# Kernel optimization log

Hardware: AMD Instinct MI355X
Metric: run time of the kernel (lower is better)

Reference implementation:

```python
import jax, jax.numpy as jnp
import numpy as np

B, N, N_IN, N_H = 8192, 16, 512, 256
NEG_ROUND = 1
MARGIN = 0.5
EPS = 1e-6  # torch F.pairwise_distance default eps


def setup_inputs() -> dict:
    key = jax.random.key(0)
    k0, k1, k2, k3 = jax.random.split(key, 4)
    seq1 = jax.random.normal(k0, (B, N, N_IN), dtype=jnp.float32)
    adj = jax.random.uniform(k1, (B, N, N), dtype=jnp.float32)
    # GCN linear (bias=False), xavier_uniform on [n_h, n_in] == same bound for [n_in, n_h]
    gx = float(np.sqrt(6.0 / (N_IN + N_H)))
    W_gcn = jax.random.uniform(k2, (N_IN, N_H), dtype=jnp.float32, minval=-gx, maxval=gx)
    b_gcn = jnp.zeros((N_H,), dtype=jnp.float32)  # Simple_GCN self.bias, init 0
    prelu_a = jnp.asarray(0.25, dtype=jnp.float32)  # nn.PReLU default
    bx = float(np.sqrt(6.0 / (N_H + N_H)))
    W_bil = jax.random.uniform(k3, (N_H, N_H), dtype=jnp.float32, minval=-bx, maxval=bx)
    b_bil = jnp.zeros((), dtype=jnp.float32)
    return {"seq1": seq1, "adj": adj, "W_gcn": W_gcn, "b_gcn": b_gcn,
            "prelu_a": prelu_a, "W_bil": W_bil, "b_bil": b_bil}


def reference(seq1, adj, W_gcn, b_gcn, prelu_a, W_bil, b_bil):
    # Simple_GCN: linear -> adjacency aggregate -> bias -> PReLU
    seq_fts = jnp.einsum('bnf,fh->bnh', seq1, W_gcn)           # [B,N,n_h]
    h1 = jnp.einsum('bnm,bmh->bnh', adj, seq_fts) + b_gcn      # bmm(adj, seq_fts)+bias
    h1 = jnp.where(h1 >= 0, h1, prelu_a * h1)                  # PReLU

    # avg readout over context nodes; last node is the target
    c = jnp.mean(h1[:, :-1, :], axis=1)                        # [B,n_h]
    h_mv = h1[:, -1, :]                                        # [B,n_h]

    def bilinear(x1, x2):  # nn.Bilinear(n_h, n_h, 1)
        return jnp.einsum('bi,ij,bj->b', x1, W_bil, x2)[:, None] + b_bil  # [B,1]

    scs = [bilinear(h_mv, c)]
    c_mi = c
    for _ in range(NEG_ROUND):  # fixed small loop, mirrors torch shift
        c_mi = jnp.concatenate([c_mi[-2:-1, :], c_mi[:-1, :]], axis=0)
        scs.append(bilinear(h_mv, c_mi))

    pos_dis = jnp.linalg.norm(h_mv - c + EPS, axis=-1)         # F.pairwise_distance
    neg_dis = jnp.linalg.norm(h_mv - c_mi + EPS, axis=-1)

    logits = jnp.concatenate(scs, axis=0)                      # [(1+NEG)*B, 1]
    # MarginRankingLoss(margin, reduction='none') with y=-1:
    # max(0, -y*(x1-x2)+margin) = max(0, (pos-neg)+margin)
    loss2 = jnp.maximum(0.0, (pos_dis - neg_dis) + MARGIN)     # [B]
    return (logits, loss2)
```

## Files before the change

kernel.cpp:

```cpp
#include <hip/hip_runtime.h>
#include <stdint.h>

typedef float f32x4 __attribute__((ext_vector_type(4)));
typedef __bf16 bfrag __attribute__((ext_vector_type(8)));
typedef unsigned short us4 __attribute__((ext_vector_type(4)));

__device__ __forceinline__ unsigned short f2bf(float f) {
  unsigned u = __float_as_uint(f);
  u += 0x7fff + ((u >> 16) & 1);
  return (unsigned short)(u >> 16);
}
__device__ __forceinline__ float bf2f(unsigned short s) {
  return __uint_as_float(((unsigned)s) << 16);
}

typedef __attribute__((address_space(3))) void lds_vp;
typedef __attribute__((address_space(1))) void gl_vp;
__device__ __forceinline__ void gload16(const void* g, void* l) {
  __builtin_amdgcn_global_load_lds((const gl_vp*)g, (lds_vp*)l, 16, 0, 0);
}

__global__ __launch_bounds__(256)
void conv_w_k(const float* __restrict__ Wg, const float* __restrict__ Wb,
              unsigned short* __restrict__ WgT, unsigned short* __restrict__ WbT) {
  int i = blockIdx.x * 256 + threadIdx.x;
  if (i < 512 * 256) { int k = i >> 8, c = i & 255; WgT[c * 512 + k] = f2bf(Wg[i]); }
  if (i < 256 * 256) { int k = i >> 8, c = i & 255; WbT[c * 256 + k] = f2bf(Wb[i]); }
}

__global__ __launch_bounds__(512, 4)
void fused1_k(const float* __restrict__ A, const unsigned short* __restrict__ Bt,
              const float* __restrict__ adj, const float* __restrict__ b_gcn,
              const float* __restrict__ prelu_a,
              float* __restrict__ Cout, float* __restrict__ Hmv) {
  __shared__ __align__(16) char sm[65536];
  const int t = threadIdx.x;
  const int lane = t & 63;
  const int wid = t >> 6;
  const int wm = wid >> 2, wn = wid & 3;
  const int lrow = lane & 15, lgrp = lane >> 4;
  const int wg = blockIdx.x;

  const float* gA = A + (size_t)(wg * 128 + (t >> 2)) * 512 + (t & 3) * 8;
  const int aw_off = t * 16;

  int aoff[4], boff[4];
#pragma unroll
  for (int m = 0; m < 4; m++) {
    int arow = wm * 64 + m * 16 + lrow;
    aoff[m] = arow * 64 + lgrp * 16;
  }
#pragma unroll
  for (int n = 0; n < 4; n++) {
    int bcol = wn * 64 + n * 16 + lrow;
    boff[n] = 8192 + bcol * 64 + ((lgrp ^ ((bcol ^ (bcol >> 2)) & 3)) << 4);
  }

  f32x4 acc[4][4];
#pragma unroll
  for (int m = 0; m < 4; m++)
#pragma unroll
    for (int n = 0; n < 4; n++) acc[m][n] = (f32x4)0.0f;

#define STAGE_B(buf, kc)                                                       \
  {                                                                            \
    _Pragma("unroll")                                                          \
    for (int i = 0; i < 2; i++) {                                              \
      int c = i * 512 + t;                                                     \
      int col = c >> 2, s = c & 3;                                             \
      int sp = s ^ ((col ^ (col >> 2)) & 3);                                   \
      gload16(Bt + (size_t)col * 512 + (kc) * 32 + sp * 8, (buf) + 8192 + c * 16); \
    }                                                                          \
  }

#define COMPUTE(cur)                                                           \
  {                                                                            \
    bfrag bf[4], af[4];                                                        \
    _Pragma("unroll")                                                          \
    for (int n = 0; n < 4; n++) bf[n] = *(const bfrag*)((cur) + boff[n]);      \
    _Pragma("unroll")                                                          \
    for (int m = 0; m < 4; m++) af[m] = *(const bfrag*)((cur) + aoff[m]);      \
    _Pragma("unroll")                                                          \
    for (int m = 0; m < 4; m++)                                                \
      _Pragma("unroll")                                                        \
      for (int n = 0; n < 4; n++)                                              \
        acc[m][n] = __builtin_amdgcn_mfma_f32_16x16x32_bf16(af[m], bf[n], acc[m][n], 0, 0, 0); \
  }

  {
    STAGE_B(sm, 0);
    f32x4 a0 = *(const f32x4*)(gA);
    f32x4 a1 = *(const f32x4*)(gA + 4);
    bfrag w;
    w[0] = (__bf16)a0.x; w[1] = (__bf16)a0.y; w[2] = (__bf16)a0.z; w[3] = (__bf16)a0.w;
    w[4] = (__bf16)a1.x; w[5] = (__bf16)a1.y; w[6] = (__bf16)a1.z; w[7] = (__bf16)a1.w;
    *(bfrag*)(sm + aw_off) = w;
    asm volatile("s_waitcnt vmcnt(0)" ::: "memory");
    asm volatile("s_waitcnt lgkmcnt(0)" ::: "memory");
    __builtin_amdgcn_s_barrier();
    asm volatile("" ::: "memory");
  }

  for (int kc = 0; kc < 15; ++kc) {
    char* cur = sm + (kc & 1) * 24576;
    char* nxt = sm + ((kc + 1) & 1) * 24576;
    f32x4 a0 = *(const f32x4*)(gA + (kc + 1) * 32);
    f32x4 a1 = *(const f32x4*)(gA + (kc + 1) * 32 + 4);
    STAGE_B(nxt, kc + 1);

    COMPUTE(cur);

    bfrag w;
    w[0] = (__bf16)a0.x; w[1] = (__bf16)a0.y; w[2] = (__bf16)a0.z; w[3] = (__bf16)a0.w;
    w[4] = (__bf16)a1.x; w[5] = (__bf16)a1.y; w[6] = (__bf16)a1.z; w[7] = (__bf16)a1.w;
    *(bfrag*)(nxt + aw_off) = w;
    asm volatile("s_waitcnt vmcnt(0)" ::: "memory");
    asm volatile("s_waitcnt lgkmcnt(0)" ::: "memory");
    __builtin_amdgcn_s_barrier();
    asm volatile("" ::: "memory");
  }
  COMPUTE(sm + 24576);
  __builtin_amdgcn_s_barrier();
  asm volatile("" ::: "memory");
#undef STAGE_B
#undef COMPUTE

  unsigned short* sf = (unsigned short*)sm;
#pragma unroll
  for (int m = 0; m < 4; m++) {
    int row = wm * 64 + m * 16 + lgrp * 4;
#pragma unroll
    for (int n = 0; n < 4; n++) {
      int col = wn * 64 + n * 16 + lrow;
#pragma unroll
      for (int rr = 0; rr < 4; rr++)
        sf[(row + rr) * 256 + col] = f2bf(acc[m][n][rr]);
    }
  }
  asm volatile("s_waitcnt lgkmcnt(0)" ::: "memory");
  __builtin_amdgcn_s_barrier();
  asm volatile("" ::: "memory");

  const float pa = prelu_a[0];
  const f32x4 bg = *(const f32x4*)(b_gcn + lane * 4);
  f32x4 sfr[16];
#pragma unroll
  for (int mm = 0; mm < 16; mm++) {
    us4 q = *(const us4*)(sf + (wid * 16 + mm) * 256 + lane * 4);
    f32x4 v;
    v.x = bf2f(q.x); v.y = bf2f(q.y); v.z = bf2f(q.z); v.w = bf2f(q.w);
    sfr[mm] = v;
  }
  const int b = wg * 8 + wid;
  const float* adjb = adj + (size_t)b * 256;
  f32x4 cacc = (f32x4)0.0f;
  f32x4 hmv = (f32x4)0.0f;
#pragma unroll
  for (int n = 0; n < 16; n++) {
    f32x4 a4 = (f32x4)0.0f;
#pragma unroll
    for (int m = 0; m < 16; m++) a4 += adjb[n * 16 + m] * sfr[m];
    a4 += bg;
    f32x4 hv;
    hv.x = a4.x >= 0.f ? a4.x : pa * a4.x;
    hv.y = a4.y >= 0.f ? a4.y : pa * a4.y;
    hv.z = a4.z >= 0.f ? a4.z : pa * a4.z;
    hv.w = a4.w >= 0.f ? a4.w : pa * a4.w;
    if (n < 15) cacc += hv; else hmv = hv;
  }
  cacc *= (1.0f / 15.0f);
  *(f32x4*)(Cout + (size_t)b * 256 + lane * 4) = cacc;
  *(f32x4*)(Hmv + (size_t)b * 256 + lane * 4) = hmv;
}

__device__ __forceinline__ void stage2(const float* __restrict__ A,
                                       const unsigned short* __restrict__ Bt,
                                       char* buf, int wg, int kc, int t) {
  {
    int c = t & 255;
    int row = c >> 3, s = c & 7;
    int sp = s ^ (((row & 3) << 1) | ((row >> 2) & 1));
    gload16(A + (size_t)(wg * 32 + row) * 256 + kc * 32 + sp * 4, buf + c * 16);
  }
#pragma unroll
  for (int i = 0; i < 2; i++) {
    int c = i * 512 + t;
    int col = c >> 2, s = c & 3;
    int sp = s ^ ((col ^ (col >> 2)) & 3);
    gload16(Bt + (size_t)col * 256 + kc * 32 + sp * 8, buf + 4096 + c * 16);
  }
}

__global__ __launch_bounds__(512)
void fused2_k(const float* __restrict__ A, const unsigned short* __restrict__ Bt,
              const float* __restrict__ C, const float* __restrict__ Hmv,
              const float* __restrict__ b_bil, float* __restrict__ out) {
  __shared__ __align__(16) char sm2[40960];
  const int t = threadIdx.x;
  const int lane = t & 63;
  const int wid = t >> 6;
  const int wm = wid >> 2, wn = wid & 3;
  const int lrow = lane & 15, lgrp = lane >> 4;
  const int wg = blockIdx.x;

  f32x4 acc[4];
#pragma unroll
  for (int n = 0; n < 4; n++) acc[n] = (f32x4)0.0f;

  stage2(A, Bt, sm2, wg, 0, t);

  for (int kc = 0; kc < 8; ++kc) {
    char* cur = sm2 + (kc & 1) * 20480;
    if (kc + 1 < 8) {
      stage2(A, Bt, sm2 + ((kc + 1) & 1) * 20480, wg, kc + 1, t);
      asm volatile("s_waitcnt vmcnt(3)" ::: "memory");
    } else {
      asm volatile("s_waitcnt vmcnt(0)" ::: "memory");
    }
    __builtin_amdgcn_s_barrier();
    asm volatile("" ::: "memory");

    bfrag bf[4];
#pragma unroll
    for (int n = 0; n < 4; n++) {
      int bcol = wn * 64 + n * 16 + lrow;
      int sB = (bcol ^ (bcol >> 2)) & 3;
      bf[n] = *(const bfrag*)(cur + 4096 + bcol * 64 + ((lgrp ^ sB) << 4));
    }
    {
      int arow = wm * 16 + lrow;
      int sw = ((arow & 3) << 1) | ((arow >> 2) & 1);
      f32x4 lo = *(const f32x4*)(cur + arow * 128 + (((lgrp * 2) ^ sw) << 4));
      f32x4 hi = *(const f32x4*)(cur + arow * 128 + (((lgrp * 2 + 1) ^ sw) << 4));
      bfrag am;
      am[0] = (__bf16)lo.x; am[1] = (__bf16)lo.y; am[2] = (__bf16)lo.z; am[3] = (__bf16)lo.w;
      am[4] = (__bf16)hi.x; am[5] = (__bf16)hi.y; am[6] = (__bf16)hi.z; am[7] = (__bf16)hi.w;
#pragma unroll
      for (int n = 0; n < 4; n++)
        acc[n] = __builtin_amdgcn_mfma_f32_16x16x32_bf16(am, bf[n], acc[n], 0, 0, 0);
    }
    __builtin_amdgcn_s_barrier();
    asm volatile("" ::: "memory");
  }

  float* sf = (float*)sm2;
  {
    int row = wm * 16 + lgrp * 4;
#pragma unroll
    for (int n = 0; n < 4; n++) {
      int col = wn * 64 + n * 16 + lrow;
#pragma unroll
      for (int rr = 0; rr < 4; rr++)
        sf[(row + rr) * 256 + col] = acc[n][rr];
    }
  }
  asm volatile("s_waitcnt lgkmcnt(0)" ::: "memory");
  __builtin_amdgcn_s_barrier();
  asm volatile("" ::: "memory");

  const float bb = b_bil[0];
#pragma unroll
  for (int r = 0; r < 4; ++r) {
    const int row = wid * 4 + r;
    const int b = wg * 32 + row;
    const int bp = (b == 0) ? 8190 : (b - 1);
    f32x4 tv = *(const f32x4*)(sf + row * 256 + lane * 4);
    f32x4 cv = *(const f32x4*)(C + (size_t)b * 256 + lane * 4);
    f32x4 cp = *(const f32x4*)(C + (size_t)bp * 256 + lane * 4);
    f32x4 hv = *(const f32x4*)(Hmv + (size_t)b * 256 + lane * 4);
    f32x4 d0 = hv - cv + 1e-6f;
    f32x4 d1 = hv - cp + 1e-6f;
    float s0 = tv.x * cv.x + tv.y * cv.y + tv.z * cv.z + tv.w * cv.w;
    float s1 = tv.x * cp.x + tv.y * cp.y + tv.z * cp.z + tv.w * cp.w;
    float p = d0.x * d0.x + d0.y * d0.y + d0.z * d0.z + d0.w * d0.w;
    float q = d1.x * d1.x + d1.y * d1.y + d1.z * d1.z + d1.w * d1.w;
#pragma unroll
    for (int m = 1; m < 64; m <<= 1) {
      s0 += __shfl_xor(s0, m, 64);
      s1 += __shfl_xor(s1, m, 64);
      p  += __shfl_xor(p, m, 64);
      q  += __shfl_xor(q, m, 64);
    }
    if (lane == 0) {
      out[b] = s0 + bb;
      out[8192 + b] = s1 + bb;
      out[16384 + b] = fmaxf(0.0f, sqrtf(p) - sqrtf(q) + 0.5f);
    }
  }
}

extern "C" void kernel_launch(void* const* d_in, const int* in_sizes, int n_in,
                              void* d_out, int out_size, void* d_ws, size_t ws_size,
                              hipStream_t stream) {
  (void)in_sizes; (void)n_in; (void)out_size; (void)ws_size;
  const float* seq1 = (const float*)d_in[0];
  const float* adj  = (const float*)d_in[1];
  const float* Wg   = (const float*)d_in[2];
  const float* bg   = (const float*)d_in[3];
  const float* pa   = (const float*)d_in[4];
  const float* Wb   = (const float*)d_in[5];
  const float* bb   = (const float*)d_in[6];
  float* out = (float*)d_out;
  char* ws = (char*)d_ws;

  unsigned short* WgT = (unsigned short*)(ws);
  unsigned short* WbT = (unsigned short*)(ws + 262144);
  float* C   = (float*)(ws + 524288);
  float* HMV = (float*)(ws + 524288 + 8388608);

  hipLaunchKernelGGL(conv_w_k, dim3(512), dim3(256), 0, stream, Wg, Wb, WgT, WbT);
  hipLaunchKernelGGL(fused1_k, dim3(1024), dim3(512), 0, stream,
                     seq1, WgT, adj, bg, pa, C, HMV);
  hipLaunchKernelGGL(fused2_k, dim3(256), dim3(512), 0, stream,
                     HMV, WbT, C, HMV, bb, out);
}
```

Baseline: 102.0 us.

## Triple-buffer GEMM K-loop with two-stage prefetch and swizzle A tile in LDS

Changes the GEMM main loop from double to triple buffering in LDS, prefetching the A and B tiles two K-steps ahead so the loop no longer waits for all outstanding global loads every iteration. It also XOR-swizzles the A tile layout in LDS to reduce bank conflicts on fragment reads, and fully unrolls the loop. The cost is more LDS per block (72KB instead of 64KB), which may cut occupancy below the four blocks per CU requested in launch bounds. The waitcnt accounting around the vmcnt counts is delicate.

```diff
diff --git a/kernel.cpp b/kernel.cpp
--- a/kernel.cpp
+++ b/kernel.cpp
@@ -33,7 +33,7 @@
               const float* __restrict__ adj, const float* __restrict__ b_gcn,
               const float* __restrict__ prelu_a,
               float* __restrict__ Cout, float* __restrict__ Hmv) {
-  __shared__ __align__(16) char sm[65536];
+  __shared__ __align__(16) char sm[73728];
   const int t = threadIdx.x;
   const int lane = t & 63;
   const int wid = t >> 6;
@@ -41,14 +41,15 @@
   const int lrow = lane & 15, lgrp = lane >> 4;
   const int wg = blockIdx.x;
 
-  const float* gA = A + (size_t)(wg * 128 + (t >> 2)) * 512 + (t & 3) * 8;
-  const int aw_off = t * 16;
+  const int arw = t >> 2;
+  const float* gA = A + (size_t)(wg * 128 + arw) * 512 + (t & 3) * 8;
+  const int awr = arw * 64 + (((t & 3) ^ ((arw >> 1) & 3)) << 4);
 
   int aoff[4], boff[4];
 #pragma unroll
   for (int m = 0; m < 4; m++) {
     int arow = wm * 64 + m * 16 + lrow;
-    aoff[m] = arow * 64 + lgrp * 16;
+    aoff[m] = arow * 64 + ((lgrp ^ ((arow >> 1) & 3)) << 4);
   }
 #pragma unroll
   for (int n = 0; n < 4; n++) {
@@ -71,6 +72,16 @@
       int sp = s ^ ((col ^ (col >> 2)) & 3);                                   \
       gload16(Bt + (size_t)col * 512 + (kc) * 32 + sp * 8, (buf) + 8192 + c * 16); \
     }                                                                          \
+  }
+
+#define CVT_WRITE_A(buf, a0, a1)                                               \
+  {                                                                            \
+    bfrag w;                                                                   \
+    w[0] = (__bf16)(a0).x; w[1] = (__bf16)(a0).y;                              \
+    w[2] = (__bf16)(a0).z; w[3] = (__bf16)(a0).w;                              \
+    w[4] = (__bf16)(a1).x; w[5] = (__bf16)(a1).y;                              \
+    w[6] = (__bf16)(a1).z; w[7] = (__bf16)(a1).w;                              \
+    *(bfrag*)((buf) + awr) = w;                                                \
   }
 
 #define COMPUTE(cur)                                                           \
@@ -88,41 +99,46 @@
   }
 
   {
+    f32x4 p0 = *(const f32x4*)(gA);
+    f32x4 p1 = *(const f32x4*)(gA + 4);
+    f32x4 q0 = *(const f32x4*)(gA + 32);
+    f32x4 q1 = *(const f32x4*)(gA + 36);
+    __builtin_amdgcn_sched_barrier(0);
     STAGE_B(sm, 0);
-    f32x4 a0 = *(const f32x4*)(gA);
-    f32x4 a1 = *(const f32x4*)(gA + 4);
-    bfrag w;
-    w[0] = (__bf16)a0.x; w[1] = (__bf16)a0.y; w[2] = (__bf16)a0.z; w[3] = (__bf16)a0.w;
-    w[4] = (__bf16)a1.x; w[5] = (__bf16)a1.y; w[6] = (__bf16)a1.z; w[7] = (__bf16)a1.w;
-    *(bfrag*)(sm + aw_off) = w;
-    asm volatile("s_waitcnt vmcnt(0)" ::: "memory");
+    STAGE_B(sm + 24576, 1);
+    __builtin_amdgcn_sched_barrier(0);
+    CVT_WRITE_A(sm, p0, p1);
+    CVT_WRITE_A(sm + 24576, q0, q1);
+    asm volatile("s_waitcnt vmcnt(2)" ::: "memory");
     asm volatile("s_waitcnt lgkmcnt(0)" ::: "memory");
     __builtin_amdgcn_s_barrier();
     asm volatile("" ::: "memory");
   }
 
-  for (int kc = 0; kc < 15; ++kc) {
-    char* cur = sm + (kc & 1) * 24576;
-    char* nxt = sm + ((kc + 1) & 1) * 24576;
-    f32x4 a0 = *(const f32x4*)(gA + (kc + 1) * 32);
-    f32x4 a1 = *(const f32x4*)(gA + (kc + 1) * 32 + 4);
-    STAGE_B(nxt, kc + 1);
-
+#pragma unroll
+  for (int kc = 0; kc < 16; ++kc) {
+    char* cur = sm + (kc % 3) * 24576;
+    char* nxt = sm + ((kc + 2) % 3) * 24576;
+    f32x4 a0, a1;
+    if (kc < 14) {
+      a0 = *(const f32x4*)(gA + (kc + 2) * 32);
+      a1 = *(const f32x4*)(gA + (kc + 2) * 32 + 4);
+      __builtin_amdgcn_sched_barrier(0);
+      STAGE_B(nxt, kc + 2);
+      __builtin_amdgcn_sched_barrier(0);
+    }
     COMPUTE(cur);
-
-    bfrag w;
-    w[0] = (__bf16)a0.x; w[1] = (__bf16)a0.y; w[2] = (__bf16)a0.z; w[3] = (__bf16)a0.w;
-    w[4] = (__bf16)a1.x; w[5] = (__bf16)a1.y; w[6] = (__bf16)a1.z; w[7] = (__bf16)a1.w;
-    *(bfrag*)(nxt + aw_off) = w;
-    asm volatile("s_waitcnt vmcnt(0)" ::: "memory");
-    asm volatile("s_waitcnt lgkmcnt(0)" ::: "memory");
+    if (kc < 14) {
+      CVT_WRITE_A(nxt, a0, a1);
+      asm volatile("s_waitcnt lgkmcnt(0)" ::: "memory");
+    } else if (kc == 14) {
+      asm volatile("s_waitcnt vmcnt(0)" ::: "memory");
+    }
     __builtin_amdgcn_s_barrier();
     asm volatile("" ::: "memory");
   }
-  COMPUTE(sm + 24576);
-  __builtin_amdgcn_s_barrier();
-  asm volatile("" ::: "memory");
 #undef STAGE_B
+#undef CVT_WRITE_A
 #undef COMPUTE
 
   unsigned short* sf = (unsigned short*)sm;
```

Measured after the change: 100.1 us, median of 2. About the same (-1.9%).

## Make fused GCN kernel persistent with direct-to-register A loads and 4-stage B pipeline

Applied to the files above, without the earlier changes.

The first fused kernel now launches 256 persistent blocks, each processing four 128-row tiles. Activations are loaded straight from global memory into registers and converted to bf16 just before the MFMAs, instead of being staged through LDS. Weight tiles go through a 4-deep LDS ring with partial vmcnt waits, and the next tile's first A chunk is prefetched across tile boundaries. The aim is to hide load latency and drop the LDS traffic for A, at the cost of 128 KB of dynamic LDS per block (one block per CU) and more register pressure.

```diff
diff --git a/kernel.cpp b/kernel.cpp
--- a/kernel.cpp
+++ b/kernel.cpp
@@ -28,12 +28,12 @@
   if (i < 256 * 256) { int k = i >> 8, c = i & 255; WbT[c * 256 + k] = f2bf(Wb[i]); }
 }
 
-__global__ __launch_bounds__(512, 4)
+__global__ __launch_bounds__(512)
 void fused1_k(const float* __restrict__ A, const unsigned short* __restrict__ Bt,
               const float* __restrict__ adj, const float* __restrict__ b_gcn,
               const float* __restrict__ prelu_a,
               float* __restrict__ Cout, float* __restrict__ Hmv) {
-  __shared__ __align__(16) char sm[65536];
+  extern __shared__ __align__(16) char sm[];
   const int t = threadIdx.x;
   const int lane = t & 63;
   const int wid = t >> 6;
@@ -41,19 +41,16 @@
   const int lrow = lane & 15, lgrp = lane >> 4;
   const int wg = blockIdx.x;
 
-  const float* gA = A + (size_t)(wg * 128 + (t >> 2)) * 512 + (t & 3) * 8;
-  const int aw_off = t * 16;
-
-  int aoff[4], boff[4];
-#pragma unroll
-  for (int m = 0; m < 4; m++) {
-    int arow = wm * 64 + m * 16 + lrow;
-    aoff[m] = arow * 64 + lgrp * 16;
-  }
+  const float* aB[4];
+#pragma unroll
+  for (int m = 0; m < 4; m++)
+    aB[m] = A + (size_t)(wm * 64 + m * 16 + lrow) * 512 + lgrp * 8;
+
+  int boff[4];
 #pragma unroll
   for (int n = 0; n < 4; n++) {
     int bcol = wn * 64 + n * 16 + lrow;
-    boff[n] = 8192 + bcol * 64 + ((lgrp ^ ((bcol ^ (bcol >> 2)) & 3)) << 4);
+    boff[n] = bcol * 64 + ((lgrp ^ ((bcol ^ (bcol >> 2)) & 3)) << 4);
   }
 
   f32x4 acc[4][4];
@@ -62,115 +59,137 @@
 #pragma unroll
     for (int n = 0; n < 4; n++) acc[m][n] = (f32x4)0.0f;
 
-#define STAGE_B(buf, kc)                                                       \
+  f32x4 afA[8], afB[8];
+
+#define STAGE_B(bufidx, kb)                                                    \
   {                                                                            \
     _Pragma("unroll")                                                          \
     for (int i = 0; i < 2; i++) {                                              \
       int c = i * 512 + t;                                                     \
       int col = c >> 2, s = c & 3;                                             \
       int sp = s ^ ((col ^ (col >> 2)) & 3);                                   \
-      gload16(Bt + (size_t)col * 512 + (kc) * 32 + sp * 8, (buf) + 8192 + c * 16); \
+      gload16(Bt + (size_t)col * 512 + (kb) * 32 + sp * 8,                     \
+              sm + (bufidx) * 16384 + c * 16);                                 \
     }                                                                          \
   }
 
-#define COMPUTE(cur)                                                           \
+#define LOAD_A(dst, tA, kb)                                                    \
   {                                                                            \
-    bfrag bf[4], af[4];                                                        \
-    _Pragma("unroll")                                                          \
-    for (int n = 0; n < 4; n++) bf[n] = *(const bfrag*)((cur) + boff[n]);      \
-    _Pragma("unroll")                                                          \
-    for (int m = 0; m < 4; m++) af[m] = *(const bfrag*)((cur) + aoff[m]);      \
+    _Pragma("unroll")                                                          \
+    for (int m = 0; m < 4; m++) {                                              \
+      const float* p_ = aB[m] + (size_t)(tA) * 65536 + (kb) * 32;              \
+      dst[2 * m]     = *(const f32x4*)(p_);                                    \
+      dst[2 * m + 1] = *(const f32x4*)(p_ + 4);                                \
+    }                                                                          \
+  }
+
+#define COMPUTE(af, bufidx)                                                    \
+  {                                                                            \
+    bfrag bf[4], am[4];                                                        \
+    _Pragma("unroll")                                                          \
+    for (int n = 0; n < 4; n++)                                                \
+      bf[n] = *(const bfrag*)(sm + (bufidx) * 16384 + boff[n]);                \
+    _Pragma("unroll")                                                          \
+    for (int m = 0; m < 4; m++) {                                              \
+      f32x4 lo = af[2 * m], hi = af[2 * m + 1];                                \
+      am[m][0] = (__bf16)lo.x; am[m][1] = (__bf16)lo.y;                        \
+      am[m][2] = (__bf16)lo.z; am[m][3] = (__bf16)lo.w;                        \
+      am[m][4] = (__bf16)hi.x; am[m][5] = (__bf16)hi.y;                        \
+      am[m][6] = (__bf16)hi.z; am[m][7] = (__bf16)hi.w;                        \
+    }                                                                          \
     _Pragma("unroll")                                                          \
     for (int m = 0; m < 4; m++)                                                \
       _Pragma("unroll")                                                        \
       for (int n = 0; n < 4; n++)                                              \
-        acc[m][n] = __builtin_amdgcn_mfma_f32_16x16x32_bf16(af[m], bf[n], acc[m][n], 0, 0, 0); \
-  }
-
-  {
-    STAGE_B(sm, 0);
-    f32x4 a0 = *(const f32x4*)(gA);
-    f32x4 a1 = *(const f32x4*)(gA + 4);
-    bfrag w;
-    w[0] = (__bf16)a0.x; w[1] = (__bf16)a0.y; w[2] = (__bf16)a0.z; w[3] = (__bf16)a0.w;
-    w[4] = (__bf16)a1.x; w[5] = (__bf16)a1.y; w[6] = (__bf16)a1.z; w[7] = (__bf16)a1.w;
-    *(bfrag*)(sm + aw_off) = w;
-    asm volatile("s_waitcnt vmcnt(0)" ::: "memory");
+        acc[m][n] = __builtin_amdgcn_mfma_f32_16x16x32_bf16(am[m], bf[n], acc[m][n], 0, 0, 0); \
+  }
+
+  STAGE_B(0, 0);
+  STAGE_B(1, 1);
+  __builtin_amdgcn_sched_barrier(0);
+  LOAD_A(afA, wg * 4, 0);
+  __builtin_amdgcn_sched_barrier(0);
+  asm volatile("s_waitcnt vmcnt(10)" ::: "memory");
+  __builtin_amdgcn_s_barrier();
+  asm volatile("" ::: "memory");
+
+  const float pa = prelu_a[0];
+  const f32x4 bg = *(const f32x4*)(b_gcn + lane * 4);
+  unsigned short* sf = (unsigned short*)(sm + 65536);
+
+  for (int mt = 0; mt < 4; ++mt) {
+    const int tile = wg * 4 + mt;
+#pragma unroll
+    for (int p = 0; p < 16; ++p) {
+      STAGE_B((p + 2) & 3, (p + 2) & 15);
+      __builtin_amdgcn_sched_barrier(0);
+      {
+        int tA = tile + (p == 15 ? 1 : 0);
+        if (tA > 1023) tA = 1023;
+        if (p & 1) { LOAD_A(afA, tA, (p + 1) & 15); }
+        else       { LOAD_A(afB, tA, (p + 1) & 15); }
+      }
+      __builtin_amdgcn_sched_barrier(0);
+      if (p & 1) { COMPUTE(afB, (p & 3)); }
+      else       { COMPUTE(afA, (p & 3)); }
+      asm volatile("s_waitcnt vmcnt(10)" ::: "memory");
+      __builtin_amdgcn_s_barrier();
+      asm volatile("" ::: "memory");
+    }
+
+#pragma unroll
+    for (int m = 0; m < 4; m++) {
+      int row = wm * 64 + m * 16 + lgrp * 4;
+#pragma unroll
+      for (int n = 0; n < 4; n++) {
+        int col = wn * 64 + n * 16 + lrow;
+#pragma unroll
+        for (int rr = 0; rr < 4; rr++)
+          sf[(row + rr) * 256 + col] = f2bf(acc[m][n][rr]);
+      }
+    }
+#pragma unroll
+    for (int m = 0; m < 4; m++)
+#pragma unroll
+      for (int n = 0; n < 4; n++) acc[m][n] = (f32x4)0.0f;
     asm volatile("s_waitcnt lgkmcnt(0)" ::: "memory");
     __builtin_amdgcn_s_barrier();
     asm volatile("" ::: "memory");
-  }
-
-  for (int kc = 0; kc < 15; ++kc) {
-    char* cur = sm + (kc & 1) * 24576;
-    char* nxt = sm + ((kc + 1) & 1) * 24576;
-    f32x4 a0 = *(const f32x4*)(gA + (kc + 1) * 32);
-    f32x4 a1 = *(const f32x4*)(gA + (kc + 1) * 32 + 4);
-    STAGE_B(nxt, kc + 1);
-
-    COMPUTE(cur);
-
-    bfrag w;
-    w[0] = (__bf16)a0.x; w[1] = (__bf16)a0.y; w[2] = (__bf16)a0.z; w[3] = (__bf16)a0.w;
-    w[4] = (__bf16)a1.x; w[5] = (__bf16)a1.y; w[6] = (__bf16)a1.z; w[7] = (__bf16)a1.w;
-    *(bfrag*)(nxt + aw_off) = w;
-    asm volatile("s_waitcnt vmcnt(0)" ::: "memory");
-    asm volatile("s_waitcnt lgkmcnt(0)" ::: "memory");
+
+    f32x4 sfr[16];
+#pragma unroll
+    for (int mm = 0; mm < 16; mm++) {
+      us4 q = *(const us4*)(sf + (wid * 16 + mm) * 256 + lane * 4);
+      f32x4 v;
+      v.x = bf2f(q.x); v.y = bf2f(q.y); v.z = bf2f(q.z); v.w = bf2f(q.w);
+      sfr[mm] = v;
+    }
+    const int b = tile * 8 + wid;
+    const float* adjb = adj + (size_t)b * 256;
+    f32x4 cacc = (f32x4)0.0f;
+    f32x4 hmv = (f32x4)0.0f;
+#pragma unroll
+    for (int n = 0; n < 16; n++) {
+      f32x4 a4 = (f32x4)0.0f;
+#pragma unroll
+      for (int m = 0; m < 16; m++) a4 += adjb[n * 16 + m] * sfr[m];
+      a4 += bg;
+      f32x4 hv;
+      hv.x = a4.x >= 0.f ? a4.x : pa * a4.x;
+      hv.y = a4.y >= 0.f ? a4.y : pa * a4.y;
+      hv.z = a4.z >= 0.f ? a4.z : pa * a4.z;
+      hv.w = a4.w >= 0.f ? a4.w : pa * a4.w;
+      if (n < 15) cacc += hv; else hmv = hv;
+    }
+    cacc *= (1.0f / 15.0f);
+    *(f32x4*)(Cout + (size_t)b * 256 + lane * 4) = cacc;
+    *(f32x4*)(Hmv + (size_t)b * 256 + lane * 4) = hmv;
     __builtin_amdgcn_s_barrier();
     asm volatile("" ::: "memory");
   }
-  COMPUTE(sm + 24576);
-  __builtin_amdgcn_s_barrier();
-  asm volatile("" ::: "memory");
 #undef STAGE_B
+#undef LOAD_A
 #undef COMPUTE
-
-  unsigned short* sf = (unsigned short*)sm;
-#pragma unroll
-  for (int m = 0; m < 4; m++) {
-    int row = wm * 64 + m * 16 + lgrp * 4;
-#pragma unroll
-    for (int n = 0; n < 4; n++) {
-      int col = wn * 64 + n * 16 + lrow;
-#pragma unroll
-      for (int rr = 0; rr < 4; rr++)
-        sf[(row + rr) * 256 + col] = f2bf(acc[m][n][rr]);
-    }
-  }
-  asm volatile("s_waitcnt lgkmcnt(0)" ::: "memory");
-  __builtin_amdgcn_s_barrier();
-  asm volatile("" ::: "memory");
-
-  const float pa = prelu_a[0];
-  const f32x4 bg = *(const f32x4*)(b_gcn + lane * 4);
-  f32x4 sfr[16];
-#pragma unroll
-  for (int mm = 0; mm < 16; mm++) {
-    us4 q = *(const us4*)(sf + (wid * 16 + mm) * 256 + lane * 4);
-    f32x4 v;
-    v.x = bf2f(q.x); v.y = bf2f(q.y); v.z = bf2f(q.z); v.w = bf2f(q.w);
-    sfr[mm] = v;
-  }
-  const int b = wg * 8 + wid;
-  const float* adjb = adj + (size_t)b * 256;
-  f32x4 cacc = (f32x4)0.0f;
-  f32x4 hmv = (f32x4)0.0f;
-#pragma unroll
-  for (int n = 0; n < 16; n++) {
-    f32x4 a4 = (f32x4)0.0f;
-#pragma unroll
-    for (int m = 0; m < 16; m++) a4 += adjb[n * 16 + m] * sfr[m];
-    a4 += bg;
-    f32x4 hv;
-    hv.x = a4.x >= 0.f ? a4.x : pa * a4.x;
-    hv.y = a4.y >= 0.f ? a4.y : pa * a4.y;
-    hv.z = a4.z >= 0.f ? a4.z : pa * a4.z;
-    hv.w = a4.w >= 0.f ? a4.w : pa * a4.w;
-    if (n < 15) cacc += hv; else hmv = hv;
-  }
-  cacc *= (1.0f / 15.0f);
-  *(f32x4*)(Cout + (size_t)b * 256 + lane * 4) = cacc;
-  *(f32x4*)(Hmv + (size_t)b * 256 + lane * 4) = hmv;
 }
 
 __device__ __forceinline__ void stage2(const float* __restrict__ A,
@@ -308,8 +327,11 @@
   float* C   = (float*)(ws + 524288);
   float* HMV = (float*)(ws + 524288 + 8388608);
 
+  (void)hipFuncSetAttribute((const void*)fused1_k,
+                            hipFuncAttributeMaxDynamicSharedMemorySize, 131072);
+
   hipLaunchKernelGGL(conv_w_k, dim3(512), dim3(256), 0, stream, Wg, Wb, WgT, WbT);
-  hipLaunchKernelGGL(fused1_k, dim3(1024), dim3(512), 0, stream,
+  hipLaunchKernelGGL(fused1_k, dim3(256), dim3(512), 131072, stream,
                      seq1, WgT, adj, bg, pa, C, HMV);
   hipLaunchKernelGGL(fused2_k, dim3(256), dim3(512), 0, stream,
                      HMV, WbT, C, HMV, bb, out);
```

Measured after the change: 190.8 us. 1.87x slower.

## Shrink GEMM1 block tile to 32 rows with 4 waves and more blocks

Applied to the files above, without the earlier changes.

The first fused GEMM kernel drops from 128-row tiles with 8 waves to 32-row tiles with 4 waves, launching 4096 blocks instead of 1024 and using less LDS per block. The A tile gets a new XOR swizzle, the loop is fully unrolled with sched_barriers, and the wait before the barrier becomes vmcnt(4) so the next B prefetch stays in flight during compute. The aim is more blocks resident at once and better latency hiding. The cost is that each block now reloads the full W_gcn slice for only 32 rows, which quadruples B traffic from L2.

```diff
diff --git a/kernel.cpp b/kernel.cpp
--- a/kernel.cpp
+++ b/kernel.cpp
@@ -2,8 +2,10 @@
 #include <stdint.h>
 
 typedef float f32x4 __attribute__((ext_vector_type(4)));
+typedef float f32x2 __attribute__((ext_vector_type(2)));
 typedef __bf16 bfrag __attribute__((ext_vector_type(8)));
 typedef unsigned short us4 __attribute__((ext_vector_type(4)));
+typedef unsigned short us2 __attribute__((ext_vector_type(2)));
 
 __device__ __forceinline__ unsigned short f2bf(float f) {
   unsigned u = __float_as_uint(f);
@@ -28,110 +30,122 @@
   if (i < 256 * 256) { int k = i >> 8, c = i & 255; WbT[c * 256 + k] = f2bf(Wb[i]); }
 }
 
-__global__ __launch_bounds__(512, 4)
+__global__ __launch_bounds__(256, 3)
 void fused1_k(const float* __restrict__ A, const unsigned short* __restrict__ Bt,
               const float* __restrict__ adj, const float* __restrict__ b_gcn,
               const float* __restrict__ prelu_a,
               float* __restrict__ Cout, float* __restrict__ Hmv) {
-  __shared__ __align__(16) char sm[65536];
+  __shared__ __align__(16) char sm[36864];
   const int t = threadIdx.x;
   const int lane = t & 63;
   const int wid = t >> 6;
-  const int wm = wid >> 2, wn = wid & 3;
   const int lrow = lane & 15, lgrp = lane >> 4;
   const int wg = blockIdx.x;
 
-  const float* gA = A + (size_t)(wg * 128 + (t >> 2)) * 512 + (t & 3) * 8;
-  const int aw_off = t * 16;
-
-  int aoff[4], boff[4];
-#pragma unroll
-  for (int m = 0; m < 4; m++) {
-    int arow = wm * 64 + m * 16 + lrow;
-    aoff[m] = arow * 64 + lgrp * 16;
+  const int arw = t >> 3;
+  const int kseg = t & 7;
+  const float* gA = A + (size_t)(wg * 32 + arw) * 512 + kseg * 4;
+  const int qrow = (arw & 3) ^ ((arw >> 2) & 3);
+  const int awr = arw * 64 + (((kseg >> 1) ^ qrow) << 4) + (kseg & 1) * 8;
+
+  int aoff[2], boff[4];
+#pragma unroll
+  for (int m = 0; m < 2; m++) {
+    int r = m * 16 + lrow;
+    int q = (r & 3) ^ ((r >> 2) & 3);
+    aoff[m] = r * 64 + ((lgrp ^ q) << 4);
   }
 #pragma unroll
   for (int n = 0; n < 4; n++) {
-    int bcol = wn * 64 + n * 16 + lrow;
-    boff[n] = 8192 + bcol * 64 + ((lgrp ^ ((bcol ^ (bcol >> 2)) & 3)) << 4);
-  }
-
-  f32x4 acc[4][4];
-#pragma unroll
-  for (int m = 0; m < 4; m++)
+    int bcol = wid * 64 + n * 16 + lrow;
+    boff[n] = 2048 + bcol * 64 + ((lgrp ^ ((bcol ^ (bcol >> 2)) & 3)) << 4);
+  }
+
+  f32x4 acc[2][4];
+#pragma unroll
+  for (int m = 0; m < 2; m++)
 #pragma unroll
     for (int n = 0; n < 4; n++) acc[m][n] = (f32x4)0.0f;
 
 #define STAGE_B(buf, kc)                                                       \
   {                                                                            \
     _Pragma("unroll")                                                          \
-    for (int i = 0; i < 2; i++) {                                              \
-      int c = i * 512 + t;                                                     \
+    for (int i = 0; i < 4; i++) {                                              \
+      int c = i * 256 + t;                                                     \
       int col = c >> 2, s = c & 3;                                             \
       int sp = s ^ ((col ^ (col >> 2)) & 3);                                   \
-      gload16(Bt + (size_t)col * 512 + (kc) * 32 + sp * 8, (buf) + 8192 + c * 16); \
+      gload16(Bt + (size_t)col * 512 + (kc) * 32 + sp * 8,                     \
+              (buf) + 2048 + c * 16);                                          \
     }                                                                          \
+  }
+
+#define STAGE_A(buf, kc)                                                       \
+  {                                                                            \
+    f32x4 av = *(const f32x4*)(gA + (kc) * 32);                                \
+    us4 w;                                                                     \
+    w.x = f2bf(av.x); w.y = f2bf(av.y); w.z = f2bf(av.z); w.w = f2bf(av.w);    \
+    *(us4*)((buf) + awr) = w;                                                  \
   }
 
 #define COMPUTE(cur)                                                           \
   {                                                                            \
-    bfrag bf[4], af[4];                                                        \
+    bfrag bf[4], af[2];                                                        \
     _Pragma("unroll")                                                          \
     for (int n = 0; n < 4; n++) bf[n] = *(const bfrag*)((cur) + boff[n]);      \
     _Pragma("unroll")                                                          \
-    for (int m = 0; m < 4; m++) af[m] = *(const bfrag*)((cur) + aoff[m]);      \
+    for (int m = 0; m < 2; m++) af[m] = *(const bfrag*)((cur) + aoff[m]);      \
     _Pragma("unroll")                                                          \
-    for (int m = 0; m < 4; m++)                                                \
+    for (int m = 0; m < 2; m++)                                                \
       _Pragma("unroll")                                                        \
       for (int n = 0; n < 4; n++)                                              \
         acc[m][n] = __builtin_amdgcn_mfma_f32_16x16x32_bf16(af[m], bf[n], acc[m][n], 0, 0, 0); \
   }
 
-  {
-    STAGE_B(sm, 0);
-    f32x4 a0 = *(const f32x4*)(gA);
-    f32x4 a1 = *(const f32x4*)(gA + 4);
-    bfrag w;
-    w[0] = (__bf16)a0.x; w[1] = (__bf16)a0.y; w[2] = (__bf16)a0.z; w[3] = (__bf16)a0.w;
-    w[4] = (__bf16)a1.x; w[5] = (__bf16)a1.y; w[6] = (__bf16)a1.z; w[7] = (__bf16)a1.w;
-    *(bfrag*)(sm + aw_off) = w;
-    asm volatile("s_waitcnt vmcnt(0)" ::: "memory");
+  STAGE_B(sm, 0);
+  STAGE_A(sm, 0);
+  asm volatile("s_waitcnt vmcnt(0)" ::: "memory");
+  asm volatile("s_waitcnt lgkmcnt(0)" ::: "memory");
+  __builtin_amdgcn_s_barrier();
+  asm volatile("" ::: "memory");
+
+#pragma unroll
+  for (int kc = 0; kc < 15; ++kc) {
+    char* cur = sm + (kc & 1) * 18432;
+    char* nxt = sm + ((kc + 1) & 1) * 18432;
+    {
+      f32x4 av = *(const f32x4*)(gA + (kc + 1) * 32);
+      __builtin_amdgcn_sched_barrier(0);
+      STAGE_B(nxt, kc + 1);
+      __builtin_amdgcn_sched_barrier(0);
+      us4 w;
+      w.x = f2bf(av.x); w.y = f2bf(av.y); w.z = f2bf(av.z); w.w = f2bf(av.w);
+      *(us4*)(nxt + awr) = w;
+    }
+    asm volatile("s_waitcnt vmcnt(4)" ::: "memory");
     asm volatile("s_waitcnt lgkmcnt(0)" ::: "memory");
     __builtin_amdgcn_s_barrier();
     asm volatile("" ::: "memory");
-  }
-
-  for (int kc = 0; kc < 15; ++kc) {
-    char* cur = sm + (kc & 1) * 24576;
-    char* nxt = sm + ((kc + 1) & 1) * 24576;
-    f32x4 a0 = *(const f32x4*)(gA + (kc + 1) * 32);
-    f32x4 a1 = *(const f32x4*)(gA + (kc + 1) * 32 + 4);
-    STAGE_B(nxt, kc + 1);
-
     COMPUTE(cur);
-
-    bfrag w;
-    w[0] = (__bf16)a0.x; w[1] = (__bf16)a0.y; w[2] = (__bf16)a0.z; w[3] = (__bf16)a0.w;
-    w[4] = (__bf16)a1.x; w[5] = (__bf16)a1.y; w[6] = (__bf16)a1.z; w[7] = (__bf16)a1.w;
-    *(bfrag*)(nxt + aw_off) = w;
-    asm volatile("s_waitcnt vmcnt(0)" ::: "memory");
-    asm volatile("s_waitcnt lgkmcnt(0)" ::: "memory");
     __builtin_amdgcn_s_barrier();
     asm volatile("" ::: "memory");
   }
-  COMPUTE(sm + 24576);
+  asm volatile("s_waitcnt vmcnt(0)" ::: "memory");
+  __builtin_amdgcn_s_barrier();
+  asm volatile("" ::: "memory");
+  COMPUTE(sm + 18432);
   __builtin_amdgcn_s_barrier();
   asm volatile("" ::: "memory");
 #undef STAGE_B
+#undef STAGE_A
 #undef COMPUTE
 
   unsigned short* sf = (unsigned short*)sm;
 #pragma unroll
-  for (int m = 0; m < 4; m++) {
-    int row = wm * 64 + m * 16 + lgrp * 4;
+  for (int m = 0; m < 2; m++) {
+    int row = m * 16 + lgrp * 4;
 #pragma unroll
     for (int n = 0; n < 4; n++) {
-      int col = wn * 64 + n * 16 + lrow;
+      int col = wid * 64 + n * 16 + lrow;
 #pragma unroll
       for (int rr = 0; rr < 4; rr++)
         sf[(row + rr) * 256 + col] = f2bf(acc[m][n][rr]);
@@ -141,36 +155,36 @@
   __builtin_amdgcn_s_barrier();
   asm volatile("" ::: "memory");
 
+  const int lb = wid >> 1;
+  const int colh = (wid & 1) * 128 + lane * 2;
   const float pa = prelu_a[0];
-  const f32x4 bg = *(const f32x4*)(b_gcn + lane * 4);
-  f32x4 sfr[16];
+  const f32x2 bg = *(const f32x2*)(b_gcn + colh);
+  f32x2 sfr[16];
 #pragma unroll
   for (int mm = 0; mm < 16; mm++) {
-    us4 q = *(const us4*)(sf + (wid * 16 + mm) * 256 + lane * 4);
-    f32x4 v;
-    v.x = bf2f(q.x); v.y = bf2f(q.y); v.z = bf2f(q.z); v.w = bf2f(q.w);
+    us2 q = *(const us2*)(sf + (lb * 16 + mm) * 256 + colh);
+    f32x2 v;
+    v.x = bf2f(q.x); v.y = bf2f(q.y);
     sfr[mm] = v;
   }
-  const int b = wg * 8 + wid;
+  const int b = wg * 2 + lb;
   const float* adjb = adj + (size_t)b * 256;
-  f32x4 cacc = (f32x4)0.0f;
-  f32x4 hmv = (f32x4)0.0f;
+  f32x2 cacc = (f32x2)0.0f;
+  f32x2 hmv = (f32x2)0.0f;
 #pragma unroll
   for (int n = 0; n < 16; n++) {
-    f32x4 a4 = (f32x4)0.0f;
-#pragma unroll
-    for (int m = 0; m < 16; m++) a4 += adjb[n * 16 + m] * sfr[m];
-    a4 += bg;
-    f32x4 hv;
-    hv.x = a4.x >= 0.f ? a4.x : pa * a4.x;
-    hv.y = a4.y >= 0.f ? a4.y : pa * a4.y;
-    hv.z = a4.z >= 0.f ? a4.z : pa * a4.z;
-    hv.w = a4.w >= 0.f ? a4.w : pa * a4.w;
+    f32x2 a2 = (f32x2)0.0f;
+#pragma unroll
+    for (int m = 0; m < 16; m++) a2 += adjb[n * 16 + m] * sfr[m];
+    a2 += bg;
+    f32x2 hv;
+    hv.x = a2.x >= 0.f ? a2.x : pa * a2.x;
+    hv.y = a2.y >= 0.f ? a2.y : pa * a2.y;
     if (n < 15) cacc += hv; else hmv = hv;
   }
   cacc *= (1.0f / 15.0f);
-  *(f32x4*)(Cout + (size_t)b * 256 + lane * 4) = cacc;
-  *(f32x4*)(Hmv + (size_t)b * 256 + lane * 4) = hmv;
+  *(f32x2*)(Cout + (size_t)b * 256 + colh) = cacc;
+  *(f32x2*)(Hmv + (size_t)b * 256 + colh) = hmv;
 }
 
 __device__ __forceinline__ void stage2(const float* __restrict__ A,
@@ -309,7 +323,7 @@
   float* HMV = (float*)(ws + 524288 + 8388608);
 
   hipLaunchKernelGGL(conv_w_k, dim3(512), dim3(256), 0, stream, Wg, Wb, WgT, WbT);
-  hipLaunchKernelGGL(fused1_k, dim3(1024), dim3(512), 0, stream,
+  hipLaunchKernelGGL(fused1_k, dim3(4096), dim3(256), 0, stream,
                      seq1, WgT, adj, bg, pa, C, HMV);
   hipLaunchKernelGGL(fused2_k, dim3(256), dim3(512), 0, stream,
                      HMV, WbT, C, HMV, bb, out);
```

After: 167.9 us. 64.6% more time.
